# Performance work log

Hardware: AMD Instinct MI355X
Metric: run time of the kernel (lower is better)

## Reference

```python
import jax, jax.numpy as jnp
import numpy as np

D_MODEL = 256
N_LEVELS = 4
N_HEADS = 4
N_POINTS = 8
D_FFN = 1024
SHAPES = [(100, 152), (50, 76), (25, 38), (13, 19)]  # (H, W) per level
BATCH = 2


def setup_inputs() -> dict:
    key = jax.random.key(0)
    ks = list(jax.random.split(key, 16))
    Len = sum(h * w for h, w in SHAPES)  # 20197
    s = 0.02

    def lin(k, fin, fout):
        k1, k2 = jax.random.split(k)
        return (jax.random.normal(k1, (fin, fout), jnp.float32) * s,
                jax.random.normal(k2, (fout,), jnp.float32) * s)

    W_off, b_off = lin(ks[0], D_MODEL, N_HEADS * N_LEVELS * N_POINTS * 2)
    W_attn, b_attn = lin(ks[1], D_MODEL, N_HEADS * N_LEVELS * N_POINTS)
    W_val, b_val = lin(ks[2], D_MODEL, D_MODEL)
    W_out, b_out = lin(ks[3], D_MODEL, D_MODEL)
    W1, b1 = lin(ks[4], D_MODEL, D_FFN)
    W2, b2 = lin(ks[5], D_FFN, D_MODEL)
    starts = np.concatenate([[0], np.cumsum([h * w for h, w in SHAPES])[:-1]])
    return {
        "src_feat": jax.random.normal(ks[6], (BATCH, Len, D_MODEL), jnp.float32),
        "reference_points": jax.random.uniform(ks[7], (BATCH, Len, N_LEVELS, 2), jnp.float32),
        "key_feat": jax.random.normal(ks[8], (BATCH, Len, D_MODEL), jnp.float32),
        "spatial_shapes": jnp.array(SHAPES, jnp.int32),
        "level_start_index": jnp.array(starts, jnp.int32),
        "W_off": W_off, "b_off": b_off, "W_attn": W_attn, "b_attn": b_attn,
        "W_val": W_val, "b_val": b_val, "W_out": W_out, "b_out": b_out,
        "W1": W1, "b1": b1, "W2": W2, "b2": b2,
        "g1": jnp.ones((D_MODEL,), jnp.float32), "be1": jnp.zeros((D_MODEL,), jnp.float32),
        "g2": jnp.ones((D_MODEL,), jnp.float32), "be2": jnp.zeros((D_MODEL,), jnp.float32),
    }


def _layernorm(x, g, b, eps=1e-5):
    mu = jnp.mean(x, -1, keepdims=True)
    var = jnp.mean(jnp.square(x - mu), -1, keepdims=True)
    return (x - mu) * jax.lax.rsqrt(var + eps) * g + b


def _bilinear(v, loc, H, W):
    # v: (N, M, H*W, D); loc: (N, M, Lq, P, 2) normalized [0,1]
    # Matches F.grid_sample(mode='bilinear', padding_mode='zeros', align_corners=False)
    x = loc[..., 0] * W - 0.5
    y = loc[..., 1] * H - 0.5
    x0 = jnp.floor(x)
    y0 = jnp.floor(y)
    wx = x - x0
    wy = y - y0
    N, M, Lq, P = x.shape
    out = None
    for dy in (0, 1):
        for dx in (0, 1):
            xi = x0 + dx
            yi = y0 + dy
            w = (wx if dx else 1.0 - wx) * (wy if dy else 1.0 - wy)
            valid = (xi >= 0) & (xi < W) & (yi >= 0) & (yi < H)
            idx = (jnp.clip(yi, 0, H - 1) * W + jnp.clip(xi, 0, W - 1)).astype(jnp.int32)
            g = jnp.take_along_axis(v, idx.reshape(N, M, Lq * P, 1), axis=2)
            g = g.reshape(N, M, Lq, P, -1) * (w * jnp.asarray(valid, v.dtype))[..., None]
            out = g if out is None else out + g
    return out  # (N, M, Lq, P, D)


def reference(src_feat, reference_points, key_feat, spatial_shapes, level_start_index,
              W_off, b_off, W_attn, b_attn, W_val, b_val, W_out, b_out,
              W1, b1, W2, b2, g1, be1, g2, be2):
    N, Lq, C = src_feat.shape
    M, L, P = N_HEADS, N_LEVELS, N_POINTS
    D = C // M
    shapes = np.asarray(spatial_shapes)  # static per-level (H, W)
    # --- MSDeformAttn ---
    value = (key_feat @ W_val + b_val).reshape(N, -1, M, D)
    off = (src_feat @ W_off + b_off).reshape(N, Lq, M, L, P, 2)
    attn = jax.nn.softmax((src_feat @ W_attn + b_attn).reshape(N, Lq, M, L * P), axis=-1)
    attn = attn.reshape(N, Lq, M, L, P)
    normalizer = jnp.stack([spatial_shapes[:, 1], spatial_shapes[:, 0]], -1).astype(src_feat.dtype)  # (L,2)=(W,H)
    loc = reference_points[:, :, None, :, None, :] + off / normalizer[None, None, None, :, None, :]
    out = jnp.zeros((N, M, Lq, D), src_feat.dtype)
    start = 0
    for l in range(L):
        H, W = int(shapes[l, 0]), int(shapes[l, 1])
        v = value[:, start:start + H * W].transpose(0, 2, 1, 3)  # (N,M,HW,D)
        samp = _bilinear(v, loc[:, :, :, l].transpose(0, 2, 1, 3, 4), H, W)  # (N,M,Lq,P,D)
        out = out + jnp.einsum('nmqpd,nqmp->nmqd', samp, attn[:, :, :, l])
        start += H * W
    out = out.transpose(0, 2, 1, 3).reshape(N, Lq, C)
    src2 = out @ W_out + b_out
    # --- residual + norm + FFN (light=False, dropout=0) ---
    x = _layernorm(src_feat + src2, g1, be1)
    ffn = jax.nn.relu(x @ W1 + b1) @ W2 + b2
    x = _layernorm(x + ffn, g2, be2)
    return (x, loc, attn)
```

## Files before the change

kernel.cpp:

```cpp
#include <hip/hip_runtime.h>
#include <hip/hip_bf16.h>

#define LQ 20197
#define NBATCH 2
#define MROWS 40394
#define MR256 ((size_t)MROWS * 256)

typedef __attribute__((ext_vector_type(8))) short bf16x8;
typedef __attribute__((ext_vector_type(4))) float f32x4;
typedef __attribute__((ext_vector_type(2))) _Float16 f16x2;

__device__ __forceinline__ unsigned short f2bf(float f) {
    unsigned u = __float_as_uint(f);
    return (unsigned short)((u + 0x7fff + ((u >> 16) & 1)) >> 16);
}
__device__ __forceinline__ float bf2f(unsigned short b) {
    return __uint_as_float((unsigned)b << 16);
}

__device__ __forceinline__ void gload16(const void* g, void* l) {
    __builtin_amdgcn_global_load_lds(
        (const __attribute__((address_space(1))) unsigned int*)g,
        (__attribute__((address_space(3))) unsigned int*)l, 16, 0, 0);
}

__device__ __forceinline__ int swz_k(int n, int kk) {
    return (kk & ~63) | (((((kk >> 3) & 7) ^ (n & 7))) << 3) | (kk & 7);
}

__global__ __launch_bounds__(256) void prep_w_k(
    const float* __restrict__ Wv, const float* __restrict__ Wo,
    const float* __restrict__ Wa, const float* __restrict__ Wu,
    const float* __restrict__ W1, const float* __restrict__ W2,
    const float* __restrict__ ba,
    unsigned short* __restrict__ BTv, unsigned short* __restrict__ BTo,
    unsigned short* __restrict__ BTa, unsigned short* __restrict__ BTu,
    unsigned short* __restrict__ BT1, unsigned short* __restrict__ BT2,
    float* __restrict__ battn)
{
    const size_t id0 = (size_t)blockIdx.x * blockDim.x + threadIdx.x;
    const size_t stride = (size_t)gridDim.x * blockDim.x;
    for (size_t i = id0; i < 65536; i += stride) {
        const int n = (int)(i >> 8), kk = (int)(i & 255);
        const int k = swz_k(n, kk);
        BTv[i] = f2bf(Wv[k * 256 + n]);
        BTo[i] = f2bf(Wo[k * 256 + n]);
        BTu[i] = f2bf(Wu[k * 256 + n]);
        BTa[i] = (n < 128) ? f2bf(Wa[k * 128 + n]) : (unsigned short)0;
    }
    for (size_t i = id0; i < 262144; i += stride) {
        const int n = (int)(i >> 8), kk = (int)(i & 255);
        BT1[i] = f2bf(W1[(size_t)swz_k(n, kk) * 1024 + n]);
        const int n2 = (int)(i >> 10), kk2 = (int)(i & 1023);
        BT2[i] = f2bf(W2[(size_t)swz_k(n2, kk2) * 256 + n2]);
    }
    if (id0 < 256) battn[id0] = (id0 < 128) ? ba[id0] : 0.f;
}

__global__ __launch_bounds__(512) void qkv_k(
    const float* __restrict__ keyf, const float* __restrict__ srcf,
    const unsigned short* __restrict__ BT012,
    const float* __restrict__ bval, const float* __restrict__ boff,
    const float* __restrict__ batt, const float* __restrict__ refpts,
    unsigned short* __restrict__ value_o, float* __restrict__ loc_o, float* __restrict__ attn_o)
{
    __shared__ __align__(16) unsigned short As[128 * 64];
    __shared__ __align__(16) unsigned short Bs[256 * 64];

    const int tid = threadIdx.x;
    const int w = tid >> 6, wr = w >> 2, wc = w & 3;
    const int l = tid & 63, lc = l & 15, rg = l >> 4;
    const int wb = tid & ~63;
    const int rowBase = blockIdx.x * 128;
    const int y = blockIdx.y;
    const float* A = (y == 0) ? keyf : srcf;
    const unsigned short* BTb = BT012 + (size_t)y * 65536;
    const float* bias = (y == 0) ? bval : (y == 1) ? boff : batt;

    f32x4 acc[4][4] = {};

    for (int k0 = 0; k0 < 256; k0 += 64) {
        if (k0) __syncthreads();
        #pragma unroll
        for (int p = 0; p < 4; ++p) {
            const int idx = tid + p * 512;
            gload16(BTb + (size_t)(idx >> 3) * 256 + k0 + (idx & 7) * 8,
                    &Bs[(p * 512 + wb) * 8]);
        }
        #pragma unroll
        for (int p = 0; p < 2; ++p) {
            const int idx = tid + p * 512;
            const int r = idx >> 3, s = idx & 7;
            const int row = rowBase + r;
            bf16x8 v = {};
            if (row < MROWS) {
                const float4 v0 = *(const float4*)(A + (size_t)row * 256 + k0 + s * 8);
                const float4 v1 = *(const float4*)(A + (size_t)row * 256 + k0 + s * 8 + 4);
                v[0] = (short)f2bf(v0.x); v[1] = (short)f2bf(v0.y);
                v[2] = (short)f2bf(v0.z); v[3] = (short)f2bf(v0.w);
                v[4] = (short)f2bf(v1.x); v[5] = (short)f2bf(v1.y);
                v[6] = (short)f2bf(v1.z); v[7] = (short)f2bf(v1.w);
            }
            *(bf16x8*)&As[r * 64 + ((s ^ (r & 7)) << 3)] = v;
        }
        __syncthreads();
        #pragma unroll
        for (int kk = 0; kk < 2; ++kk) {
            bf16x8 aF[4], bF[4];
            const int sl = kk * 4 + rg;
            #pragma unroll
            for (int i = 0; i < 4; ++i) {
                const int r = wr * 64 + i * 16 + lc;
                aF[i] = *(const bf16x8*)&As[r * 64 + ((sl ^ (r & 7)) << 3)];
            }
            #pragma unroll
            for (int j = 0; j < 4; ++j) {
                const int n = wc * 64 + j * 16 + lc;
                bF[j] = *(const bf16x8*)&Bs[n * 64 + ((sl ^ (n & 7)) << 3)];
            }
            #pragma unroll
            for (int i = 0; i < 4; ++i)
                #pragma unroll
                for (int j = 0; j < 4; ++j)
                    acc[i][j] = __builtin_amdgcn_mfma_f32_16x16x32_bf16(aF[i], bF[j], acc[i][j], 0, 0, 0);
        }
    }

    if (y == 0) {
        #pragma unroll
        for (int i = 0; i < 4; ++i)
            #pragma unroll
            for (int r4 = 0; r4 < 4; ++r4) {
                const int row = rowBase + wr * 64 + i * 16 + rg * 4 + r4;
                if (row >= MROWS) continue;
                #pragma unroll
                for (int j = 0; j < 4; ++j) {
                    const int col = wc * 64 + j * 16 + lc;
                    const _Float16 h = (_Float16)(acc[i][j][r4] + bias[col]);
                    value_o[(size_t)row * 256 + col] = __builtin_bit_cast(unsigned short, h);
                }
            }
    } else if (y == 1) {
        const float INV[8] = {1.f/152, 1.f/100, 1.f/76, 1.f/50, 1.f/38, 1.f/25, 1.f/19, 1.f/13};
        #pragma unroll
        for (int i = 0; i < 4; ++i)
            #pragma unroll
            for (int r4 = 0; r4 < 4; ++r4) {
                const int row = rowBase + wr * 64 + i * 16 + rg * 4 + r4;
                if (row >= MROWS) continue;
                #pragma unroll
                for (int j = 0; j < 4; ++j) {
                    const int col = wc * 64 + j * 16 + lc;
                    const int lvl = (col >> 4) & 3, xy = col & 1;
                    const float off = acc[i][j][r4] + bias[col];
                    const float ref = refpts[(size_t)row * 8 + lvl * 2 + xy];
                    loc_o[(size_t)row * 256 + col] = ref + off * INV[lvl * 2 + xy];
                }
            }
    } else {
        if (wc >= 2) return;
        #pragma unroll
        for (int i = 0; i < 4; ++i)
            #pragma unroll
            for (int r4 = 0; r4 < 4; ++r4) {
                const int row = rowBase + wr * 64 + i * 16 + rg * 4 + r4;
                float v[4];
                #pragma unroll
                for (int j = 0; j < 4; ++j) v[j] = acc[i][j][r4] + bias[wc * 64 + j * 16 + lc];
                float mA = fmaxf(v[0], v[1]), mB = fmaxf(v[2], v[3]);
                #pragma unroll
                for (int o = 1; o <= 8; o <<= 1) {
                    mA = fmaxf(mA, __shfl_xor(mA, o));
                    mB = fmaxf(mB, __shfl_xor(mB, o));
                }
                float e[4];
                e[0] = __expf(v[0] - mA); e[1] = __expf(v[1] - mA);
                e[2] = __expf(v[2] - mB); e[3] = __expf(v[3] - mB);
                float sA = e[0] + e[1], sB = e[2] + e[3];
                #pragma unroll
                for (int o = 1; o <= 8; o <<= 1) {
                    sA += __shfl_xor(sA, o);
                    sB += __shfl_xor(sB, o);
                }
                if (row >= MROWS) continue;
                #pragma unroll
                for (int j = 0; j < 4; ++j) {
                    const int col = wc * 64 + j * 16 + lc;
                    attn_o[(size_t)row * 128 + col] = e[j] / (j < 2 ? sA : sB);
                }
            }
    }
}

__global__ __launch_bounds__(512) void ffn1_k(
    const unsigned short* __restrict__ Ap, const unsigned short* __restrict__ BT,
    const float* __restrict__ bias, unsigned short* __restrict__ h0,
    unsigned short* __restrict__ h1)
{
    __shared__ __align__(16) unsigned short As[128 * 64];
    __shared__ __align__(16) unsigned short Bs[256 * 64];

    const int tid = threadIdx.x;
    const int w = tid >> 6, wr = w >> 2, wc = w & 3;
    const int l = tid & 63, lc = l & 15, rg = l >> 4;
    const int wb = tid & ~63;
    const int rowBase = blockIdx.x * 128;
    const unsigned short* BTb = BT + (size_t)blockIdx.y * 65536;
    const bool fullA = (rowBase + 128 <= MROWS);

    f32x4 acc[4][4] = {};

    for (int k0 = 0; k0 < 256; k0 += 64) {
        if (k0) __syncthreads();
        #pragma unroll
        for (int p = 0; p < 4; ++p) {
            const int idx = tid + p * 512;
            gload16(BTb + (size_t)(idx >> 3) * 256 + k0 + (idx & 7) * 8,
                    &Bs[(p * 512 + wb) * 8]);
        }
        if (fullA) {
            #pragma unroll
            for (int p = 0; p < 2; ++p) {
                const int idx = tid + p * 512;
                gload16(Ap + (size_t)(rowBase + (idx >> 3)) * 256 + k0 + (idx & 7) * 8,
                        &As[(p * 512 + wb) * 8]);
            }
        } else {
            #pragma unroll
            for (int p = 0; p < 2; ++p) {
                const int idx = tid + p * 512;
                const int row = rowBase + (idx >> 3);
                bf16x8 v = {};
                if (row < MROWS)
                    v = *(const bf16x8*)(Ap + (size_t)row * 256 + k0 + (idx & 7) * 8);
                *(bf16x8*)&As[idx * 8] = v;
            }
        }
        __syncthreads();
        #pragma unroll
        for (int kk = 0; kk < 2; ++kk) {
            bf16x8 aF[4], bF[4];
            const int sl = kk * 4 + rg;
            #pragma unroll
            for (int i = 0; i < 4; ++i) {
                const int r = wr * 64 + i * 16 + lc;
                aF[i] = *(const bf16x8*)&As[r * 64 + ((sl ^ (r & 7)) << 3)];
            }
            #pragma unroll
            for (int j = 0; j < 4; ++j) {
                const int n = wc * 64 + j * 16 + lc;
                bF[j] = *(const bf16x8*)&Bs[n * 64 + ((sl ^ (n & 7)) << 3)];
            }
            #pragma unroll
            for (int i = 0; i < 4; ++i)
                #pragma unroll
                for (int j = 0; j < 4; ++j)
                    acc[i][j] = __builtin_amdgcn_mfma_f32_16x16x32_bf16(aF[i], bF[j], acc[i][j], 0, 0, 0);
        }
    }

    #pragma unroll
    for (int i = 0; i < 4; ++i)
        #pragma unroll
        for (int r4 = 0; r4 < 4; ++r4) {
            const int row = rowBase + wr * 64 + i * 16 + rg * 4 + r4;
            if (row >= MROWS) continue;
            #pragma unroll
            for (int j = 0; j < 4; ++j) {
                const int colg = blockIdx.y * 256 + wc * 64 + j * 16 + lc;
                const float t = fmaxf(acc[i][j][r4] + bias[colg], 0.f);
                unsigned short* hb = (colg < 512) ? h0 : h1;
                const int lcol = colg & 511;
                const int gg = lcol >> 3, e = lcol & 7;
                const int gs = (gg & 56) | ((gg & 7) ^ (row & 7));
                hb[(size_t)row * 512 + gs * 8 + e] = f2bf(t);
            }
        }
}

__global__ __launch_bounds__(256) void ln1_k(
    const unsigned short* __restrict__ Ap, const unsigned short* __restrict__ BT,
    const float* __restrict__ bias, const float* __restrict__ aux,
    const float* __restrict__ g, const float* __restrict__ be,
    unsigned short* __restrict__ out)
{
    __shared__ __align__(16) unsigned short As[64 * 64];
    __shared__ __align__(16) unsigned short Bs[256 * 64];
    __shared__ float ps[64][4], pq[64][4];
    __shared__ float mu_s[64], rs_s[64];

    const int tid = threadIdx.x;
    const int l = tid & 63, w = tid >> 6;
    const int lc = l & 15, rg = l >> 4;
    const int rowBase = blockIdx.x * 64;
    const int wb = tid & ~63;
    const bool fullA = (rowBase + 64 <= MROWS);

    f32x4 acc[4][4] = {};

    for (int k0 = 0; k0 < 256; k0 += 64) {
        if (k0) __syncthreads();
        #pragma unroll
        for (int p = 0; p < 8; ++p) {
            const int idx = tid + p * 256;
            gload16(BT + (size_t)(idx >> 3) * 256 + k0 + (idx & 7) * 8,
                    &Bs[(p * 256 + wb) * 8]);
        }
        if (fullA) {
            #pragma unroll
            for (int p = 0; p < 2; ++p) {
                const int idx = tid + p * 256;
                gload16(Ap + (size_t)(rowBase + (idx >> 3)) * 256 + k0 + (idx & 7) * 8,
                        &As[(p * 256 + wb) * 8]);
            }
        } else {
            #pragma unroll
            for (int p = 0; p < 2; ++p) {
                const int idx = tid + p * 256;
                const int row = rowBase + (idx >> 3);
                bf16x8 v = {};
                if (row < MROWS)
                    v = *(const bf16x8*)(Ap + (size_t)row * 256 + k0 + (idx & 7) * 8);
                *(bf16x8*)&As[idx * 8] = v;
            }
        }
        __syncthreads();
        #pragma unroll
        for (int kk = 0; kk < 2; ++kk) {
            bf16x8 aF[4], bF[4];
            const int sl = kk * 4 + rg;
            #pragma unroll
            for (int i = 0; i < 4; ++i) {
                const int r = i * 16 + lc;
                aF[i] = *(const bf16x8*)&As[r * 64 + ((sl ^ (r & 7)) << 3)];
            }
            #pragma unroll
            for (int j = 0; j < 4; ++j) {
                const int n = w * 64 + j * 16 + lc;
                bF[j] = *(const bf16x8*)&Bs[n * 64 + ((sl ^ (n & 7)) << 3)];
            }
            #pragma unroll
            for (int i = 0; i < 4; ++i)
                #pragma unroll
                for (int j = 0; j < 4; ++j)
                    acc[i][j] = __builtin_amdgcn_mfma_f32_16x16x32_bf16(aF[i], bF[j], acc[i][j], 0, 0, 0);
        }
    }

    #pragma unroll
    for (int i = 0; i < 4; ++i)
        #pragma unroll
        for (int r4 = 0; r4 < 4; ++r4) {
            const int row = rowBase + i * 16 + rg * 4 + r4;
            float s = 0.f, q = 0.f;
            #pragma unroll
            for (int j = 0; j < 4; ++j) {
                const int col = w * 64 + j * 16 + lc;
                float t = acc[i][j][r4] + bias[col];
                if (row < MROWS) t += aux[(size_t)row * 256 + col];
                acc[i][j][r4] = t;
                s += t; q += t * t;
            }
            #pragma unroll
            for (int o = 1; o <= 8; o <<= 1) { s += __shfl_xor(s, o); q += __shfl_xor(q, o); }
            if (lc == 0) { ps[i * 16 + rg * 4 + r4][w] = s; pq[i * 16 + rg * 4 + r4][w] = q; }
        }
    __syncthreads();
    if (tid < 64) {
        const float s = ps[tid][0] + ps[tid][1] + ps[tid][2] + ps[tid][3];
        const float q = pq[tid][0] + pq[tid][1] + pq[tid][2] + pq[tid][3];
        const float m = s * (1.f / 256.f);
        mu_s[tid] = m;
        rs_s[tid] = rsqrtf(q * (1.f / 256.f) - m * m + 1e-5f);
    }
    __syncthreads();
    #pragma unroll
    for (int i = 0; i < 4; ++i)
        #pragma unroll
        for (int r4 = 0; r4 < 4; ++r4) {
            const int rl = i * 16 + rg * 4 + r4;
            const int row = rowBase + rl;
            if (row >= MROWS) continue;
            const float m = mu_s[rl], r = rs_s[rl];
            #pragma unroll
            for (int j = 0; j < 4; ++j) {
                const int col = w * 64 + j * 16 + lc;
                const int gg = col >> 3, e = col & 7;
                const int gs = (gg & 24) | ((gg & 7) ^ (row & 7));
                out[(size_t)row * 256 + gs * 8 + e] = f2bf((acc[i][j][r4] - m) * r * g[col] + be[col]);
            }
        }
}

__global__ __launch_bounds__(256) void ffn2_k(
    const unsigned short* __restrict__ h0, const unsigned short* __restrict__ h1,
    const unsigned short* __restrict__ BT2,
    const float* __restrict__ bias, const unsigned short* __restrict__ xb,
    const float* __restrict__ g, const float* __restrict__ be,
    float* __restrict__ out)
{
    __shared__ __align__(16) unsigned short As[64 * 64];
    __shared__ __align__(16) unsigned short Bs[256 * 64];
    __shared__ float ps[64][4], pq[64][4];
    __shared__ float mu_s[64], rs_s[64];

    const int tid = threadIdx.x;
    const int l = tid & 63, w = tid >> 6;
    const int lc = l & 15, rg = l >> 4;
    const int rowBase = blockIdx.x * 64;
    const int wb = tid & ~63;
    const bool fullA = (rowBase + 64 <= MROWS);

    f32x4 acc[4][4] = {};

    for (int kc = 0; kc < 16; ++kc) {
        if (kc) __syncthreads();
        #pragma unroll
        for (int p = 0; p < 8; ++p) {
            const int idx = tid + p * 256;
            gload16(BT2 + (size_t)(idx >> 3) * 1024 + kc * 64 + (idx & 7) * 8,
                    &Bs[(p * 256 + wb) * 8]);
        }
        const unsigned short* Ab = (kc < 8) ? h0 : h1;
        const int koff = (kc & 7) * 64;
        if (fullA) {
            #pragma unroll
            for (int p = 0; p < 2; ++p) {
                const int idx = tid + p * 256;
                gload16(Ab + (size_t)(rowBase + (idx >> 3)) * 512 + koff + (idx & 7) * 8,
                        &As[(p * 256 + wb) * 8]);
            }
        } else {
            #pragma unroll
            for (int p = 0; p < 2; ++p) {
                const int idx = tid + p * 256;
                const int row = rowBase + (idx >> 3);
                bf16x8 v = {};
                if (row < MROWS) v = *(const bf16x8*)(Ab + (size_t)row * 512 + koff + (idx & 7) * 8);
                *(bf16x8*)&As[idx * 8] = v;
            }
        }
        __syncthreads();
        #pragma unroll
        for (int kk = 0; kk < 2; ++kk) {
            bf16x8 aF[4], bF[4];
            const int sl = kk * 4 + rg;
            #pragma unroll
            for (int i = 0; i < 4; ++i) {
                const int r = i * 16 + lc;
                aF[i] = *(const bf16x8*)&As[r * 64 + ((sl ^ (r & 7)) << 3)];
            }
            #pragma unroll
            for (int j = 0; j < 4; ++j) {
                const int n = w * 64 + j * 16 + lc;
                bF[j] = *(const bf16x8*)&Bs[n * 64 + ((sl ^ (n & 7)) << 3)];
            }
            #pragma unroll
            for (int i = 0; i < 4; ++i)
                #pragma unroll
                for (int j = 0; j < 4; ++j)
                    acc[i][j] = __builtin_amdgcn_mfma_f32_16x16x32_bf16(aF[i], bF[j], acc[i][j], 0, 0, 0);
        }
    }

    #pragma unroll
    for (int i = 0; i < 4; ++i)
        #pragma unroll
        for (int r4 = 0; r4 < 4; ++r4) {
            const int row = rowBase + i * 16 + rg * 4 + r4;
            float s = 0.f, q = 0.f;
            #pragma unroll
            for (int j = 0; j < 4; ++j) {
                const int col = w * 64 + j * 16 + lc;
                float t = acc[i][j][r4] + bias[col];
                if (row < MROWS) {
                    const int gg = col >> 3, e = col & 7;
                    const int gs = (gg & 24) | ((gg & 7) ^ (row & 7));
                    t += bf2f(xb[(size_t)row * 256 + gs * 8 + e]);
                }
                acc[i][j][r4] = t;
                s += t; q += t * t;
            }
            #pragma unroll
            for (int o = 1; o <= 8; o <<= 1) { s += __shfl_xor(s, o); q += __shfl_xor(q, o); }
            if (lc == 0) { ps[i * 16 + rg * 4 + r4][w] = s; pq[i * 16 + rg * 4 + r4][w] = q; }
        }
    __syncthreads();
    if (tid < 64) {
        const float s = ps[tid][0] + ps[tid][1] + ps[tid][2] + ps[tid][3];
        const float q = pq[tid][0] + pq[tid][1] + pq[tid][2] + pq[tid][3];
        const float m = s * (1.f / 256.f);
        mu_s[tid] = m;
        rs_s[tid] = rsqrtf(q * (1.f / 256.f) - m * m + 1e-5f);
    }
    __syncthreads();
    #pragma unroll
    for (int i = 0; i < 4; ++i)
        #pragma unroll
        for (int r4 = 0; r4 < 4; ++r4) {
            const int rl = i * 16 + rg * 4 + r4;
            const int row = rowBase + rl;
            if (row >= MROWS) continue;
            const float m = mu_s[rl], r = rs_s[rl];
            #pragma unroll
            for (int j = 0; j < 4; ++j) {
                const int col = w * 64 + j * 16 + lc;
                out[(size_t)row * 256 + col] = (acc[i][j][r4] - m) * r * g[col] + be[col];
            }
        }
}

#define QB2 8
__global__ __launch_bounds__(256, 8) void sample_k(
    const unsigned short* __restrict__ value, const float* __restrict__ loc_i,
    const float* __restrict__ attn_i, unsigned short* __restrict__ samp_o)
{
    constexpr int LVL_H[4] = {100, 50, 25, 13};
    constexpr int LVL_W[4] = {152, 76, 38, 19};
    constexpr int LVL_S[4] = {0, 15200, 19000, 19950};
    const int tid = threadIdx.x;

    const int nwg = gridDim.x;
    const int bid = blockIdx.x;
    const int xcd = bid & 7, lid = bid >> 3;
    const int qq = nwg >> 3, rr = nwg & 7;
    const int sw = (xcd < rr ? xcd * (qq + 1) : rr * (qq + 1) + (xcd - rr) * qq) + lid;
    const int rowBase = sw * QB2;

    __shared__ unsigned sU[QB2][4][33][4];

    #pragma unroll
    for (int it = 0; it < 4; ++it) {
        const int item = tid + it * 256;
        const int qs = item >> 7;
        const int t  = item & 127;
        const int row = rowBase + qs;
        if (row < MROWS) {
            const int lv = (t >> 3) & 3;
            const int n = (row >= LQ) ? 1 : 0;
            const int H = LVL_H[lv], W = LVL_W[lv];
            const float lx = loc_i[(size_t)row * 256 + t * 2 + 0];
            const float ly = loc_i[(size_t)row * 256 + t * 2 + 1];
            const float a  = attn_i[(size_t)row * 128 + t];
            const float x = lx * (float)W - 0.5f;
            const float y = ly * (float)H - 0.5f;
            const float x0f = floorf(x), y0f = floorf(y);
            const float wx = x - x0f, wy = y - y0f;
            const int x0 = (int)x0f, y0 = (int)y0f;
            const int base = n * LQ + LVL_S[lv];
            unsigned e[4];
            #pragma unroll
            for (int nb = 0; nb < 4; ++nb) {
                const int dx = nb & 1, dy = nb >> 1;
                const int xi = x0 + dx, yi = y0 + dy;
                const bool valid = (xi >= 0) & (xi < W) & (yi >= 0) & (yi < H);
                const float wgt = (dx ? wx : 1.f - wx) * (dy ? wy : 1.f - wy) * a;
                const int xc = min(max(xi, 0), W - 1);
                const int yc = min(max(yi, 0), H - 1);
                const unsigned pos = (unsigned)(base + yc * W + xc);
                const _Float16 hw = (_Float16)(valid ? wgt : 0.f);
                e[nb] = (pos << 16) | (unsigned)__builtin_bit_cast(unsigned short, hw);
            }
            *(uint4*)&sU[qs][t >> 5][t & 31][0] = make_uint4(e[0], e[1], e[2], e[3]);
        }
    }
    __syncthreads();

    const int qs = tid >> 5;
    const int c8 = tid & 31;
    const int row = rowBase + qs;
    if (row >= MROWS) return;
    const int m = c8 >> 3;
    const char* vb = (const char*)value + c8 * 16;

    f16x2 A0 = {0, 0}, A1 = {0, 0}, A2 = {0, 0}, A3 = {0, 0};
    #pragma unroll 4
    for (int j = 0; j < 64; ++j) {
        const int t0 = j >> 1, np = (j & 1) << 1;
        const uint2 uu = *(const uint2*)&sU[qs][m][t0][np];
        {
            const unsigned u = uu.x;
            const unsigned off = (u >> 16) << 9;
            const unsigned w2u = __builtin_amdgcn_perm(u, u, 0x01000100);
            const f16x2 w2 = __builtin_bit_cast(f16x2, w2u);
            const uint4 vv = *(const uint4*)(vb + off);
            A0 = __builtin_elementwise_fma(__builtin_bit_cast(f16x2, vv.x), w2, A0);
            A1 = __builtin_elementwise_fma(__builtin_bit_cast(f16x2, vv.y), w2, A1);
            A2 = __builtin_elementwise_fma(__builtin_bit_cast(f16x2, vv.z), w2, A2);
            A3 = __builtin_elementwise_fma(__builtin_bit_cast(f16x2, vv.w), w2, A3);
        }
        {
            const unsigned u = uu.y;
            const unsigned off = (u >> 16) << 9;
            const unsigned w2u = __builtin_amdgcn_perm(u, u, 0x01000100);
            const f16x2 w2 = __builtin_bit_cast(f16x2, w2u);
            const uint4 vv = *(const uint4*)(vb + off);
            A0 = __builtin_elementwise_fma(__builtin_bit_cast(f16x2, vv.x), w2, A0);
            A1 = __builtin_elementwise_fma(__builtin_bit_cast(f16x2, vv.y), w2, A1);
            A2 = __builtin_elementwise_fma(__builtin_bit_cast(f16x2, vv.z), w2, A2);
            A3 = __builtin_elementwise_fma(__builtin_bit_cast(f16x2, vv.w), w2, A3);
        }
    }
    uint4 o;
    o.x = (unsigned)f2bf((float)A0.x) | ((unsigned)f2bf((float)A0.y) << 16);
    o.y = (unsigned)f2bf((float)A1.x) | ((unsigned)f2bf((float)A1.y) << 16);
    o.z = (unsigned)f2bf((float)A2.x) | ((unsigned)f2bf((float)A2.y) << 16);
    o.w = (unsigned)f2bf((float)A3.x) | ((unsigned)f2bf((float)A3.y) << 16);
    const int slot = (c8 & 24) | ((c8 & 7) ^ (row & 7));
    *(uint4*)(samp_o + (size_t)row * 256 + slot * 8) = o;
}

extern "C" void kernel_launch(void* const* d_in, const int* in_sizes, int n_in,
                              void* d_out, int out_size, void* d_ws, size_t ws_size,
                              hipStream_t stream)
{
    const float* src_feat = (const float*)d_in[0];
    const float* refpts   = (const float*)d_in[1];
    const float* key_feat = (const float*)d_in[2];
    const float* W_off  = (const float*)d_in[5];
    const float* b_off  = (const float*)d_in[6];
    const float* W_attn = (const float*)d_in[7];
    const float* b_attn = (const float*)d_in[8];
    const float* W_val  = (const float*)d_in[9];
    const float* b_val  = (const float*)d_in[10];
    const float* W_out  = (const float*)d_in[11];
    const float* b_out  = (const float*)d_in[12];
    const float* W1  = (const float*)d_in[13];
    const float* b1  = (const float*)d_in[14];
    const float* W2  = (const float*)d_in[15];
    const float* b2  = (const float*)d_in[16];
    const float* g1  = (const float*)d_in[17];
    const float* be1 = (const float*)d_in[18];
    const float* g2  = (const float*)d_in[19];
    const float* be2 = (const float*)d_in[20];

    float* out = (float*)d_out;
    float* x_out    = out;
    float* loc_out  = out + MR256;
    float* attn_out = out + 2 * MR256;

    char* ws = (char*)d_ws;
    unsigned short* BTv   = (unsigned short*)(ws + 0);
    unsigned short* BTo   = (unsigned short*)(ws + 131072);
    unsigned short* BTa   = (unsigned short*)(ws + 262144);
    unsigned short* BTu   = (unsigned short*)(ws + 393216);
    unsigned short* BT1   = (unsigned short*)(ws + 524288);
    unsigned short* BT2   = (unsigned short*)(ws + 1048576);
    float*          battn = (float*)(ws + 1572864);
    unsigned short* value = (unsigned short*)(ws + 2097152);
    unsigned short* samp  = (unsigned short*)(ws + 2097152 + MR256 * 2);
    unsigned short* xb    = (unsigned short*)(ws + 2097152 + MR256 * 4);
    unsigned short* h0    = value;
    unsigned short* h1    = (unsigned short*)x_out;

    const int RB  = (MROWS + 63) / 64;
    const int RB2 = (MROWS + 127) / 128;

    prep_w_k<<<512, 256, 0, stream>>>(W_val, W_off, W_attn, W_out, W1, W2, b_attn,
                                      BTv, BTo, BTa, BTu, BT1, BT2, battn);
    qkv_k<<<dim3(RB2, 3), 512, 0, stream>>>(key_feat, src_feat, BTv,
                                            b_val, b_off, battn, refpts,
                                            value, loc_out, attn_out);
    sample_k<<<(MROWS + QB2 - 1) / QB2, 256, 0, stream>>>(value, loc_out, attn_out, samp);
    ln1_k<<<RB, 256, 0, stream>>>(samp, BTu, b_out, src_feat, g1, be1, xb);
    ffn1_k<<<dim3(RB2, 4), 512, 0, stream>>>(xb, BT1, b1, h0, h1);
    ffn2_k<<<RB, 256, 0, stream>>>(h0, h1, BT2, b2, xb, g2, be2, x_out);
}
```

Baseline: 315.4 us.

## Double-buffer LDS tiles in ln1 and ffn2 GEMM kernels

Both the LayerNorm-fused GEMM kernels (ln1_k and ffn2_k) now keep two LDS buffers per operand and issue the global->LDS loads for the next K chunk before running the MFMA on the current one. This hides load latency behind compute and drops one barrier per iteration. The LN reduction scratch arrays now alias the first A buffer, which keeps LDS from growing further. LDS use roughly doubles to about 80KB per block, which may cut occupancy.

Result: slower. 332.6 us (+5.5%).

```diff
diff --git a/kernel.cpp b/kernel.cpp
--- a/kernel.cpp
+++ b/kernel.cpp
@@ -284,10 +284,12 @@
     const float* __restrict__ g, const float* __restrict__ be,
     unsigned short* __restrict__ out)
 {
-    __shared__ __align__(16) unsigned short As[64 * 64];
-    __shared__ __align__(16) unsigned short Bs[256 * 64];
-    __shared__ float ps[64][4], pq[64][4];
-    __shared__ float mu_s[64], rs_s[64];
+    __shared__ __align__(16) unsigned short As[2][64 * 64];
+    __shared__ __align__(16) unsigned short Bs[2][256 * 64];
+    float (*ps)[4] = (float (*)[4])(&As[0][0]);
+    float (*pq)[4] = (float (*)[4])(&As[0][1024]);
+    float* mu_s = (float*)(&As[0][2048]);
+    float* rs_s = (float*)(&As[0][2304]);
 
     const int tid = threadIdx.x;
     const int l = tid & 63, w = tid >> 6;
@@ -296,22 +298,19 @@
     const int wb = tid & ~63;
     const bool fullA = (rowBase + 64 <= MROWS);
 
-    f32x4 acc[4][4] = {};
-
-    for (int k0 = 0; k0 < 256; k0 += 64) {
-        if (k0) __syncthreads();
+    auto stage = [&](int k0, int b) {
         #pragma unroll
         for (int p = 0; p < 8; ++p) {
             const int idx = tid + p * 256;
             gload16(BT + (size_t)(idx >> 3) * 256 + k0 + (idx & 7) * 8,
-                    &Bs[(p * 256 + wb) * 8]);
+                    &Bs[b][(p * 256 + wb) * 8]);
         }
         if (fullA) {
             #pragma unroll
             for (int p = 0; p < 2; ++p) {
                 const int idx = tid + p * 256;
                 gload16(Ap + (size_t)(rowBase + (idx >> 3)) * 256 + k0 + (idx & 7) * 8,
-                        &As[(p * 256 + wb) * 8]);
+                        &As[b][(p * 256 + wb) * 8]);
             }
         } else {
             #pragma unroll
@@ -321,10 +320,18 @@
                 bf16x8 v = {};
                 if (row < MROWS)
                     v = *(const bf16x8*)(Ap + (size_t)row * 256 + k0 + (idx & 7) * 8);
-                *(bf16x8*)&As[idx * 8] = v;
-            }
-        }
-        __syncthreads();
+                *(bf16x8*)&As[b][idx * 8] = v;
+            }
+        }
+    };
+
+    f32x4 acc[4][4] = {};
+    stage(0, 0);
+    __syncthreads();
+
+    for (int ks = 0; ks < 4; ++ks) {
+        const int b = ks & 1;
+        if (ks < 3) stage((ks + 1) * 64, b ^ 1);
         #pragma unroll
         for (int kk = 0; kk < 2; ++kk) {
             bf16x8 aF[4], bF[4];
@@ -332,12 +339,12 @@
             #pragma unroll
             for (int i = 0; i < 4; ++i) {
                 const int r = i * 16 + lc;
-                aF[i] = *(const bf16x8*)&As[r * 64 + ((sl ^ (r & 7)) << 3)];
+                aF[i] = *(const bf16x8*)&As[b][r * 64 + ((sl ^ (r & 7)) << 3)];
             }
             #pragma unroll
             for (int j = 0; j < 4; ++j) {
                 const int n = w * 64 + j * 16 + lc;
-                bF[j] = *(const bf16x8*)&Bs[n * 64 + ((sl ^ (n & 7)) << 3)];
+                bF[j] = *(const bf16x8*)&Bs[b][n * 64 + ((sl ^ (n & 7)) << 3)];
             }
             #pragma unroll
             for (int i = 0; i < 4; ++i)
@@ -345,6 +352,7 @@
                 for (int j = 0; j < 4; ++j)
                     acc[i][j] = __builtin_amdgcn_mfma_f32_16x16x32_bf16(aF[i], bF[j], acc[i][j], 0, 0, 0);
         }
+        __syncthreads();
     }
 
     #pragma unroll
@@ -399,10 +407,12 @@
     const float* __restrict__ g, const float* __restrict__ be,
     float* __restrict__ out)
 {
-    __shared__ __align__(16) unsigned short As[64 * 64];
-    __shared__ __align__(16) unsigned short Bs[256 * 64];
-    __shared__ float ps[64][4], pq[64][4];
-    __shared__ float mu_s[64], rs_s[64];
+    __shared__ __align__(16) unsigned short As[2][64 * 64];
+    __shared__ __align__(16) unsigned short Bs[2][256 * 64];
+    float (*ps)[4] = (float (*)[4])(&As[0][0]);
+    float (*pq)[4] = (float (*)[4])(&As[0][1024]);
+    float* mu_s = (float*)(&As[0][2048]);
+    float* rs_s = (float*)(&As[0][2304]);
 
     const int tid = threadIdx.x;
     const int l = tid & 63, w = tid >> 6;
@@ -411,15 +421,12 @@
     const int wb = tid & ~63;
     const bool fullA = (rowBase + 64 <= MROWS);
 
-    f32x4 acc[4][4] = {};
-
-    for (int kc = 0; kc < 16; ++kc) {
-        if (kc) __syncthreads();
+    auto stage = [&](int kc, int b) {
         #pragma unroll
         for (int p = 0; p < 8; ++p) {
             const int idx = tid + p * 256;
             gload16(BT2 + (size_t)(idx >> 3) * 1024 + kc * 64 + (idx & 7) * 8,
-                    &Bs[(p * 256 + wb) * 8]);
+                    &Bs[b][(p * 256 + wb) * 8]);
         }
         const unsigned short* Ab = (kc < 8) ? h0 : h1;
         const int koff = (kc & 7) * 64;
@@ -428,7 +435,7 @@
             for (int p = 0; p < 2; ++p) {
                 const int idx = tid + p * 256;
                 gload16(Ab + (size_t)(rowBase + (idx >> 3)) * 512 + koff + (idx & 7) * 8,
-                        &As[(p * 256 + wb) * 8]);
+                        &As[b][(p * 256 + wb) * 8]);
             }
         } else {
             #pragma unroll
@@ -436,11 +443,20 @@
                 const int idx = tid + p * 256;
                 const int row = rowBase + (idx >> 3);
                 bf16x8 v = {};
-                if (row < MROWS) v = *(const bf16x8*)(Ab + (size_t)row * 512 + koff + (idx & 7) * 8);
-                *(bf16x8*)&As[idx * 8] = v;
-            }
-        }
-        __syncthreads();
+                if (row < MROWS)
+                    v = *(const bf16x8*)(Ab + (size_t)row * 512 + koff + (idx & 7) * 8);
+                *(bf16x8*)&As[b][idx * 8] = v;
+            }
+        }
+    };
+
+    f32x4 acc[4][4] = {};
+    stage(0, 0);
+    __syncthreads();
+
+    for (int kc = 0; kc < 16; ++kc) {
+        const int b = kc & 1;
+        if (kc < 15) stage(kc + 1, b ^ 1);
         #pragma unroll
         for (int kk = 0; kk < 2; ++kk) {
             bf16x8 aF[4], bF[4];
@@ -448,12 +464,12 @@
             #pragma unroll
             for (int i = 0; i < 4; ++i) {
                 const int r = i * 16 + lc;
-                aF[i] = *(const bf16x8*)&As[r * 64 + ((sl ^ (r & 7)) << 3)];
+                aF[i] = *(const bf16x8*)&As[b][r * 64 + ((sl ^ (r & 7)) << 3)];
             }
             #pragma unroll
             for (int j = 0; j < 4; ++j) {
                 const int n = w * 64 + j * 16 + lc;
-                bF[j] = *(const bf16x8*)&Bs[n * 64 + ((sl ^ (n & 7)) << 3)];
+                bF[j] = *(const bf16x8*)&Bs[b][n * 64 + ((sl ^ (n & 7)) << 3)];
             }
             #pragma unroll
             for (int i = 0; i < 4; ++i)
@@ -461,6 +477,7 @@
                 for (int j = 0; j < 4; ++j)
                     acc[i][j] = __builtin_amdgcn_mfma_f32_16x16x32_bf16(aF[i], bF[j], acc[i][j], 0, 0, 0);
         }
+        __syncthreads();
     }
 
     #pragma unroll
```
